# Performance work log

Measured on AMD Instinct MI355X. Metric: run time of the kernel, lower is better.

The kernel has to match this reference:

```python
import jax, jax.numpy as jnp
import numpy as np

N, E, IN, HID, OUT, H = 10000, 320000, 256, 128, 128, 4
SLOPE = 0.2

def setup_inputs() -> dict:
    key = jax.random.key(0)
    ks = jax.random.split(key, 12)
    s = lambda d: 1.0 / np.sqrt(d)
    return {
        "x": jax.random.normal(ks[0], (N, IN), jnp.float32),
        "edge_index": jax.random.randint(ks[1], (2, E), 0, N, jnp.int32),
        "W1": jax.random.normal(ks[2], (IN, H * HID), jnp.float32) * s(IN),
        "a_src1": jax.random.normal(ks[3], (H, HID), jnp.float32) * s(HID),
        "a_dst1": jax.random.normal(ks[4], (H, HID), jnp.float32) * s(HID),
        "b1": jnp.zeros((H * HID,), jnp.float32),
        "W2": jax.random.normal(ks[5], (H * HID, H * OUT), jnp.float32) * s(H * HID),
        "a_src2": jax.random.normal(ks[6], (H, OUT), jnp.float32) * s(OUT),
        "a_dst2": jax.random.normal(ks[7], (H, OUT), jnp.float32) * s(OUT),
        "b2": jnp.zeros((OUT,), jnp.float32),
    }

def _gat_layer(x, src, dst, W, a_src, a_dst, bias, concat, C):
    n = x.shape[0]
    h = (x @ W).reshape(n, H, C)                      # [N,H,C]
    alpha_s = jnp.einsum('nhc,hc->nh', h, a_src)      # [N,H]
    alpha_d = jnp.einsum('nhc,hc->nh', h, a_dst)
    e = jax.nn.leaky_relu(alpha_s[src] + alpha_d[dst], SLOPE)  # [E,H]
    # segment softmax over incoming edges of each dst node
    m = jax.ops.segment_max(e, dst, num_segments=n)   # [N,H]
    m = jnp.where(jnp.isfinite(m), m, 0.0)
    ex = jnp.exp(e - m[dst])
    denom = jax.ops.segment_sum(ex, dst, num_segments=n)
    alpha = ex / (denom[dst] + 1e-16)                 # [E,H]
    msg = h[src] * alpha[:, :, None]                  # [E,H,C]
    out = jax.ops.segment_sum(msg, dst, num_segments=n)  # [N,H,C]
    out = out.reshape(n, H * C) if concat else out.mean(axis=1)
    return out + bias

def reference(x, edge_index, W1, a_src1, a_dst1, b1, W2, a_src2, a_dst2, b2):
    n = x.shape[0]
    loops = jnp.arange(n, dtype=edge_index.dtype)
    src = jnp.concatenate([edge_index[0], loops])
    dst = jnp.concatenate([edge_index[1], loops])
    h = _gat_layer(x, src, dst, W1, a_src1, a_dst1, b1, True, HID)
    h = jax.nn.relu(h)  # dropout is identity in eval mode
    out = _gat_layer(h, src, dst, W2, a_src2, a_dst2, b2, False, OUT)
    return out
```

## Files before the change

### kernel.cpp

```cpp
#include <hip/hip_runtime.h>
#include <hip/hip_fp16.h>
#include <math.h>

#define Nn 10000
#define Ee 320000
#define EE 330000
#define INF_ 256
#define NH 4
#define OUTC 128
#define F1 512
#define F2 512
#define SLOPE 0.2f
#define STRIDE 80
#define LDK 72
#define MT 157

#define TP1_BLOCKS 32
#define TP2_BLOCKS 64
#define ZC_BLOCKS 40
#define P1_GRID (TP1_BLOCKS + ZC_BLOCKS)
#define GEMM_TILES 640
#define SCAT_BLOCKS 430
#define G1_GRID (GEMM_TILES + SCAT_BLOCKS + TP2_BLOCKS)

static __device__ __forceinline__ float lrelu(float x) { return fmaxf(x, SLOPE * x); }

using frag_ab = __attribute__((ext_vector_type(8))) _Float16;
using frag_c  = __attribute__((ext_vector_type(4))) float;

static __device__ __forceinline__ void tile_decode(int bid, int& m, int& h) {
    int m8 = bid & 7, rest = bid >> 3;
    h = rest & 3;
    m = (rest >> 2) * 8 + m8;
}

__global__ __launch_bounds__(256) void prep_w1(int* counts, const float* __restrict__ W1,
                                               _Float16* __restrict__ w1t) {
    __shared__ _Float16 tile[64 * 65];
    int b = blockIdx.x, t = threadIdx.x;
    if (b < TP1_BLOCKS) {
        int k0 = (b >> 3) * 64, n0 = (b & 7) * 64;
        int cl = t & 63, rw = t >> 6;
#pragma unroll
        for (int it = 0; it < 16; it++) {
            int r = it * 4 + rw;
            tile[cl * 65 + r] = (_Float16)W1[(size_t)(k0 + r) * F1 + n0 + cl];
        }
        __syncthreads();
#pragma unroll
        for (int it = 0; it < 16; it++) {
            int nl = it * 4 + rw;
            w1t[(size_t)(n0 + nl) * INF_ + k0 + cl] = tile[nl * 65 + cl];
        }
    } else {
        int i = (b - TP1_BLOCKS) * 256 + t;
        if (i < Nn) counts[i] = 0;
    }
}

template <bool AF32>
static __device__ void gemm_tile(const _Float16* __restrict__ Ah,
                                 const float* __restrict__ Af,
                                 const _Float16* __restrict__ BT,
                                 _Float16* __restrict__ C,
                                 const float* __restrict__ a_src,
                                 const float* __restrict__ a_dst,
                                 float* __restrict__ as_out,
                                 float* __restrict__ ad_out,
                                 int K, int bmi, int head,
                                 _Float16* As, _Float16* Bs) {
    const int tid = threadIdx.x;
    const int wave = tid >> 6, lane = tid & 63;
    const int q = lane >> 4, ml = lane & 15;
    const int bm = bmi * 64, bn = head * 128;
    const int srow = tid >> 2, scol = (tid & 3) * 16;

    frag_c acc[8];
#pragma unroll
    for (int f = 0; f < 8; f++)
#pragma unroll
        for (int r = 0; r < 4; r++) acc[f][r] = 0.f;

    for (int k0 = 0; k0 < K; k0 += 64) {
        int gm = bm + srow;
        frag_ab av0, av1;
        if (gm < Nn) {
            if constexpr (AF32) {
                const float* Ap = Af + (size_t)gm * K + k0 + scol;
                float4 v0 = *(const float4*)Ap;
                float4 v1 = *(const float4*)(Ap + 4);
                float4 v2 = *(const float4*)(Ap + 8);
                float4 v3 = *(const float4*)(Ap + 12);
                av0[0] = (_Float16)v0.x; av0[1] = (_Float16)v0.y;
                av0[2] = (_Float16)v0.z; av0[3] = (_Float16)v0.w;
                av0[4] = (_Float16)v1.x; av0[5] = (_Float16)v1.y;
                av0[6] = (_Float16)v1.z; av0[7] = (_Float16)v1.w;
                av1[0] = (_Float16)v2.x; av1[1] = (_Float16)v2.y;
                av1[2] = (_Float16)v2.z; av1[3] = (_Float16)v2.w;
                av1[4] = (_Float16)v3.x; av1[5] = (_Float16)v3.y;
                av1[6] = (_Float16)v3.z; av1[7] = (_Float16)v3.w;
            } else {
                av0 = *(const frag_ab*)(Ah + (size_t)gm * K + k0 + scol);
                av1 = *(const frag_ab*)(Ah + (size_t)gm * K + k0 + scol + 8);
            }
        } else {
#pragma unroll
            for (int j = 0; j < 8; j++) { av0[j] = (_Float16)0.f; av1[j] = (_Float16)0.f; }
        }
        frag_ab b00 = *(const frag_ab*)(BT + (size_t)(bn + srow) * K + k0 + scol);
        frag_ab b01 = *(const frag_ab*)(BT + (size_t)(bn + srow) * K + k0 + scol + 8);
        frag_ab b10 = *(const frag_ab*)(BT + (size_t)(bn + 64 + srow) * K + k0 + scol);
        frag_ab b11 = *(const frag_ab*)(BT + (size_t)(bn + 64 + srow) * K + k0 + scol + 8);

        *(frag_ab*)&As[srow * LDK + scol]     = av0;
        *(frag_ab*)&As[srow * LDK + scol + 8] = av1;
        *(frag_ab*)&Bs[srow * LDK + scol]     = b00;
        *(frag_ab*)&Bs[srow * LDK + scol + 8] = b01;
        *(frag_ab*)&Bs[(64 + srow) * LDK + scol]     = b10;
        *(frag_ab*)&Bs[(64 + srow) * LDK + scol + 8] = b11;
        __syncthreads();
        frag_ab a0 = *(frag_ab*)&As[(wave * 16 + ml) * LDK + q * 8];
        frag_ab a1 = *(frag_ab*)&As[(wave * 16 + ml) * LDK + 32 + q * 8];
#pragma unroll
        for (int f = 0; f < 8; f++) {
            frag_ab bl = *(frag_ab*)&Bs[(f * 16 + ml) * LDK + q * 8];
            acc[f] = __builtin_amdgcn_mfma_f32_16x16x32_f16(a0, bl, acc[f], 0, 0, 0);
            frag_ab bh = *(frag_ab*)&Bs[(f * 16 + ml) * LDK + 32 + q * 8];
            acc[f] = __builtin_amdgcn_mfma_f32_16x16x32_f16(a1, bh, acc[f], 0, 0, 0);
        }
        __syncthreads();
    }
    float asum[4] = {}, dsum[4] = {};
#pragma unroll
    for (int f = 0; f < 8; f++) {
        int cl = f * 16 + ml;
        int col = bn + cl;
        float sa = a_src[head * 128 + cl];
        float da = a_dst[head * 128 + cl];
#pragma unroll
        for (int r = 0; r < 4; r++) {
            int row = bm + wave * 16 + q * 4 + r;
            if (row < Nn) C[(size_t)row * (NH * 128) + col] = (_Float16)acc[f][r];
            asum[r] += acc[f][r] * sa;
            dsum[r] += acc[f][r] * da;
        }
    }
#pragma unroll
    for (int r = 0; r < 4; r++) {
#pragma unroll
        for (int off = 1; off < 16; off <<= 1) {
            asum[r] += __shfl_xor(asum[r], off);
            dsum[r] += __shfl_xor(dsum[r], off);
        }
    }
    if (ml == 0) {
#pragma unroll
        for (int r = 0; r < 4; r++) {
            int row = bm + wave * 16 + q * 4 + r;
            if (row < Nn) {
                as_out[(size_t)head * Nn + row] = asum[r];
                ad_out[(size_t)head * Nn + row] = dsum[r];
            }
        }
    }
}

__global__ __launch_bounds__(256) void gemm1_scatter(const float* __restrict__ x,
                                                     const _Float16* __restrict__ w1t,
                                                     _Float16* __restrict__ hh,
                                                     const float* __restrict__ a_src,
                                                     const float* __restrict__ a_dst,
                                                     float* __restrict__ as_out,
                                                     float* __restrict__ ad_out,
                                                     const int* __restrict__ ei,
                                                     int* counts, int* __restrict__ csr,
                                                     const float* __restrict__ W2,
                                                     _Float16* __restrict__ w2t) {
    __shared__ _Float16 As[64 * LDK];
    __shared__ _Float16 Bs[128 * LDK];
    int bid = blockIdx.x;
    int t = threadIdx.x;
    if (bid < GEMM_TILES) {
        int m, h;
        tile_decode(bid, m, h);
        if (m < MT)
            gemm_tile<true>(nullptr, x, w1t, hh, a_src, a_dst, as_out, ad_out,
                            INF_, m, h, As, Bs);
    } else if (bid < GEMM_TILES + SCAT_BLOCKS) {
        int bi = bid - GEMM_TILES;
        for (int e = bi * 256 + t; e < EE; e += SCAT_BLOCKS * 256) {
            int src, dst;
            if (e < Ee) { src = ei[e]; dst = ei[Ee + e]; }
            else        { src = e - Ee; dst = e - Ee; }
            int slot = atomicAdd(&counts[dst], 1);
            if (slot < STRIDE) csr[dst * STRIDE + slot] = src;
        }
    } else {
        int bb = bid - GEMM_TILES - SCAT_BLOCKS;
        int k0 = (bb >> 3) * 64, n0 = (bb & 7) * 64;
        int cl = t & 63, r4 = t >> 6;
        _Float16* tile = As;
#pragma unroll
        for (int it = 0; it < 16; it++) {
            int r = it * 4 + r4;
            tile[cl * 65 + r] = (_Float16)W2[(size_t)(k0 + r) * F2 + n0 + cl];
        }
        __syncthreads();
#pragma unroll
        for (int it = 0; it < 16; it++) {
            int nl = it * 4 + r4;
            w2t[(size_t)(n0 + nl) * F1 + k0 + cl] = tile[nl * 65 + cl];
        }
    }
}

__global__ __launch_bounds__(256) void gemm2(const _Float16* __restrict__ aggh,
                                             const _Float16* __restrict__ w2t,
                                             _Float16* __restrict__ hh,
                                             const float* __restrict__ a_src,
                                             const float* __restrict__ a_dst,
                                             float* __restrict__ as_out,
                                             float* __restrict__ ad_out) {
    __shared__ _Float16 As[64 * LDK];
    __shared__ _Float16 Bs[128 * LDK];
    int m, h;
    tile_decode(blockIdx.x, m, h);
    if (m < MT)
        gemm_tile<false>(aggh, nullptr, w2t, hh, a_src, a_dst, as_out, ad_out,
                         F1, m, h, As, Bs);
}

__global__ __launch_bounds__(256) void passAB1(const int* __restrict__ counts,
                                               const int* __restrict__ csr,
                                               const float* __restrict__ as,
                                               const float* __restrict__ ad,
                                               const _Float16* __restrict__ hh,
                                               const float* __restrict__ b1,
                                               _Float16* __restrict__ agg) {
    __shared__ int2 ew[16][84];
    int head = blockIdx.x & 3;
    int qw = threadIdx.x >> 4;
    int l = threadIdx.x & 15;
    int n = (blockIdx.x >> 2) * 16 + qw;
    int deg = counts[n]; if (deg > STRIDE) deg = STRIDE;
    int pdeg = (deg + 7) & ~7;
    const float* ash = as + (size_t)head * Nn;
    float adh = ad[(size_t)head * Nn + n];
    int base = n * STRIDE;
    float s = 0.f;
    for (int k = l; k < pdeg; k += 16) {
        int src = 0; float e = 0.f;
        if (k < deg) {
            src = csr[base + k];
            e = __expf(lrelu(ash[src] + adh));
        }
        ew[qw][k] = make_int2(src, __float_as_int(e));
        s += e;
    }
    s += __shfl_xor(s, 1);
    s += __shfl_xor(s, 2);
    s += __shfl_xor(s, 4);
    s += __shfl_xor(s, 8);
    float inv = 1.f / (s + 1e-16f);
    int c = head * 128 + (l << 3);
    float acc[8] = {};
    for (int kk = 0; kk < pdeg; kk += 8) {
        int2 pj[8];
#pragma unroll
        for (int j = 0; j < 8; j++) pj[j] = ew[qw][kk + j];
#pragma unroll
        for (int j = 0; j < 8; j++) {
            float w = __int_as_float(pj[j].y);
            frag_ab r = *(const frag_ab*)(hh + (size_t)pj[j].x * F1 + c);
#pragma unroll
            for (int u = 0; u < 8; u++) acc[u] = fmaf((float)r[u], w, acc[u]);
        }
    }
    _Float16 oh[8];
#pragma unroll
    for (int j = 0; j < 8; j++)
        oh[j] = (_Float16)fmaxf(acc[j] * inv + b1[c + j], 0.f);
    *(float4*)&agg[(size_t)n * F1 + c] = *(float4*)oh;
}

__global__ __launch_bounds__(256) void passAB2(const int* __restrict__ counts,
                                               const int* __restrict__ csr,
                                               const float* __restrict__ as,
                                               const float* __restrict__ ad,
                                               const _Float16* __restrict__ hh,
                                               _Float16* __restrict__ tmp) {
    __shared__ int2 ew[16][84];
    int head = blockIdx.x & 3;
    int qw = threadIdx.x >> 4;
    int l = threadIdx.x & 15;
    int n = (blockIdx.x >> 2) * 16 + qw;
    int deg = counts[n]; if (deg > STRIDE) deg = STRIDE;
    int pdeg = (deg + 7) & ~7;
    const float* ash = as + (size_t)head * Nn;
    float adh = ad[(size_t)head * Nn + n];
    int base = n * STRIDE;
    float s = 0.f;
    for (int k = l; k < pdeg; k += 16) {
        int src = 0; float e = 0.f;
        if (k < deg) {
            src = csr[base + k];
            e = __expf(lrelu(ash[src] + adh));
        }
        ew[qw][k] = make_int2(src, __float_as_int(e));
        s += e;
    }
    s += __shfl_xor(s, 1);
    s += __shfl_xor(s, 2);
    s += __shfl_xor(s, 4);
    s += __shfl_xor(s, 8);
    float inv = 1.f / (s + 1e-16f);
    int c = head * 128 + (l << 3);
    float acc[8] = {};
    for (int kk = 0; kk < pdeg; kk += 8) {
        int2 pj[8];
#pragma unroll
        for (int j = 0; j < 8; j++) pj[j] = ew[qw][kk + j];
#pragma unroll
        for (int j = 0; j < 8; j++) {
            float w = __int_as_float(pj[j].y);
            frag_ab r = *(const frag_ab*)(hh + (size_t)pj[j].x * F2 + c);
#pragma unroll
            for (int u = 0; u < 8; u++) acc[u] = fmaf((float)r[u], w, acc[u]);
        }
    }
    float qq = 0.25f * inv;
    _Float16 oh[8];
#pragma unroll
    for (int j = 0; j < 8; j++) oh[j] = (_Float16)(acc[j] * qq);
    *(float4*)&tmp[(size_t)n * F2 + c] = *(float4*)oh;
}

__global__ void reduce4(const _Float16* __restrict__ tmp, const float* __restrict__ b2,
                        float* __restrict__ out) {
    int i = blockIdx.x * 256 + threadIdx.x;
    if (i >= Nn * OUTC) return;
    int n = i >> 7, oc = i & 127;
    const _Float16* tp = tmp + (size_t)n * 512 + oc;
    out[i] = (float)tp[0] + (float)tp[128] + (float)tp[256] + (float)tp[384] + b2[oc];
}

extern "C" void kernel_launch(void* const* d_in, const int* in_sizes, int n_in,
                              void* d_out, int out_size, void* d_ws, size_t ws_size,
                              hipStream_t stream) {
    const float* x      = (const float*)d_in[0];
    const int*   ei     = (const int*)d_in[1];
    const float* W1     = (const float*)d_in[2];
    const float* a_src1 = (const float*)d_in[3];
    const float* a_dst1 = (const float*)d_in[4];
    const float* b1     = (const float*)d_in[5];
    const float* W2     = (const float*)d_in[6];
    const float* a_src2 = (const float*)d_in[7];
    const float* a_dst2 = (const float*)d_in[8];
    const float* b2     = (const float*)d_in[9];
    float* out = (float*)d_out;

    char* w = (char*)d_ws;
    _Float16* hh   = (_Float16*)w; w += (size_t)Nn * F1 * 2;
    _Float16* aggh = (_Float16*)w; w += (size_t)Nn * F1 * 2;
    _Float16* tmp  = (_Float16*)w; w += (size_t)Nn * F2 * 2;
    _Float16* w1t  = (_Float16*)w; w += (size_t)F1 * INF_ * 2;
    _Float16* w2t  = (_Float16*)w; w += (size_t)F2 * F1 * 2;
    float* as1     = (float*)w;    w += (size_t)NH * Nn * 4;
    float* ad1     = (float*)w;    w += (size_t)NH * Nn * 4;
    float* as2     = (float*)w;    w += (size_t)NH * Nn * 4;
    float* ad2     = (float*)w;    w += (size_t)NH * Nn * 4;
    int* csr       = (int*)w;      w += (size_t)Nn * STRIDE * 4;
    int* counts    = (int*)w;      w += (size_t)Nn * 4;

    prep_w1<<<P1_GRID, 256, 0, stream>>>(counts, W1, w1t);

    gemm1_scatter<<<G1_GRID, 256, 0, stream>>>(x, w1t, hh, a_src1, a_dst1, as1, ad1,
                                               ei, counts, csr, W2, w2t);
    passAB1<<<(Nn / 16) * NH, 256, 0, stream>>>(counts, csr, as1, ad1, hh, b1, aggh);

    gemm2<<<GEMM_TILES, 256, 0, stream>>>(aggh, w2t, hh, a_src2, a_dst2, as2, ad2);
    passAB2<<<(Nn / 16) * NH, 256, 0, stream>>>(counts, csr, as2, ad2, hh, tmp);
    reduce4<<<(Nn * OUTC + 255) / 256, 256, 0, stream>>>(tmp, b2, out);
}
```

Baseline: 176.7 us.

## Load GEMM MFMA fragments directly from global memory, dropping LDS staging

Each wave now reads its A and B MFMA fragments straight from global memory into registers instead of staging 64x64 tiles in shared memory. This removes both __syncthreads per k-step and frees LDS. K becomes a template parameter so the k-loop can fully unroll. In exchange, all four waves load the same B tile separately and the reads are less coalesced, which raises global/L2 traffic.

```diff
diff --git a/kernel.cpp b/kernel.cpp
--- a/kernel.cpp
+++ b/kernel.cpp
@@ -12,7 +12,6 @@
 #define F2 512
 #define SLOPE 0.2f
 #define STRIDE 80
-#define LDK 72
 #define MT 157
 
 #define TP1_BLOCKS 32
@@ -58,7 +57,7 @@
     }
 }
 
-template <bool AF32>
+template <bool AF32, int K>
 static __device__ void gemm_tile(const _Float16* __restrict__ Ah,
                                  const float* __restrict__ Af,
                                  const _Float16* __restrict__ BT,
@@ -67,13 +66,11 @@
                                  const float* __restrict__ a_dst,
                                  float* __restrict__ as_out,
                                  float* __restrict__ ad_out,
-                                 int K, int bmi, int head,
-                                 _Float16* As, _Float16* Bs) {
+                                 int bmi, int head) {
     const int tid = threadIdx.x;
     const int wave = tid >> 6, lane = tid & 63;
     const int q = lane >> 4, ml = lane & 15;
     const int bm = bmi * 64, bn = head * 128;
-    const int srow = tid >> 2, scol = (tid & 3) * 16;
 
     frag_c acc[8];
 #pragma unroll
@@ -81,55 +78,46 @@
 #pragma unroll
         for (int r = 0; r < 4; r++) acc[f][r] = 0.f;
 
+    const int arow = bm + wave * 16 + ml;
+    const bool rowok = arow < Nn;
+    const float*    Apf = AF32 ? (Af + (size_t)arow * K + q * 8) : nullptr;
+    const _Float16* Aph = AF32 ? nullptr : (Ah + (size_t)arow * K + q * 8);
+    const _Float16* Bp  = BT + (size_t)(bn + ml) * K + q * 8;
+
+#pragma unroll
     for (int k0 = 0; k0 < K; k0 += 64) {
-        int gm = bm + srow;
-        frag_ab av0, av1;
-        if (gm < Nn) {
+        frag_ab a0, a1;
+        if (rowok) {
             if constexpr (AF32) {
-                const float* Ap = Af + (size_t)gm * K + k0 + scol;
-                float4 v0 = *(const float4*)Ap;
-                float4 v1 = *(const float4*)(Ap + 4);
-                float4 v2 = *(const float4*)(Ap + 8);
-                float4 v3 = *(const float4*)(Ap + 12);
-                av0[0] = (_Float16)v0.x; av0[1] = (_Float16)v0.y;
-                av0[2] = (_Float16)v0.z; av0[3] = (_Float16)v0.w;
-                av0[4] = (_Float16)v1.x; av0[5] = (_Float16)v1.y;
-                av0[6] = (_Float16)v1.z; av0[7] = (_Float16)v1.w;
-                av1[0] = (_Float16)v2.x; av1[1] = (_Float16)v2.y;
-                av1[2] = (_Float16)v2.z; av1[3] = (_Float16)v2.w;
-                av1[4] = (_Float16)v3.x; av1[5] = (_Float16)v3.y;
-                av1[6] = (_Float16)v3.z; av1[7] = (_Float16)v3.w;
+                float4 v0 = *(const float4*)(Apf + k0);
+                float4 v1 = *(const float4*)(Apf + k0 + 4);
+                float4 v2 = *(const float4*)(Apf + k0 + 32);
+                float4 v3 = *(const float4*)(Apf + k0 + 36);
+                a0[0] = (_Float16)v0.x; a0[1] = (_Float16)v0.y;
+                a0[2] = (_Float16)v0.z; a0[3] = (_Float16)v0.w;
+                a0[4] = (_Float16)v1.x; a0[5] = (_Float16)v1.y;
+                a0[6] = (_Float16)v1.z; a0[7] = (_Float16)v1.w;
+                a1[0] = (_Float16)v2.x; a1[1] = (_Float16)v2.y;
+                a1[2] = (_Float16)v2.z; a1[3] = (_Float16)v2.w;
+                a1[4] = (_Float16)v3.x; a1[5] = (_Float16)v3.y;
+                a1[6] = (_Float16)v3.z; a1[7] = (_Float16)v3.w;
             } else {
-                av0 = *(const frag_ab*)(Ah + (size_t)gm * K + k0 + scol);
-                av1 = *(const frag_ab*)(Ah + (size_t)gm * K + k0 + scol + 8);
+                a0 = *(const frag_ab*)(Aph + k0);
+                a1 = *(const frag_ab*)(Aph + k0 + 32);
             }
         } else {
 #pragma unroll
-            for (int j = 0; j < 8; j++) { av0[j] = (_Float16)0.f; av1[j] = (_Float16)0.f; }
-        }
-        frag_ab b00 = *(const frag_ab*)(BT + (size_t)(bn + srow) * K + k0 + scol);
-        frag_ab b01 = *(const frag_ab*)(BT + (size_t)(bn + srow) * K + k0 + scol + 8);
-        frag_ab b10 = *(const frag_ab*)(BT + (size_t)(bn + 64 + srow) * K + k0 + scol);
-        frag_ab b11 = *(const frag_ab*)(BT + (size_t)(bn + 64 + srow) * K + k0 + scol + 8);
-
-        *(frag_ab*)&As[srow * LDK + scol]     = av0;
-        *(frag_ab*)&As[srow * LDK + scol + 8] = av1;
-        *(frag_ab*)&Bs[srow * LDK + scol]     = b00;
-        *(frag_ab*)&Bs[srow * LDK + scol + 8] = b01;
-        *(frag_ab*)&Bs[(64 + srow) * LDK + scol]     = b10;
-        *(frag_ab*)&Bs[(64 + srow) * LDK + scol + 8] = b11;
-        __syncthreads();
-        frag_ab a0 = *(frag_ab*)&As[(wave * 16 + ml) * LDK + q * 8];
-        frag_ab a1 = *(frag_ab*)&As[(wave * 16 + ml) * LDK + 32 + q * 8];
+            for (int j = 0; j < 8; j++) { a0[j] = (_Float16)0.f; a1[j] = (_Float16)0.f; }
+        }
 #pragma unroll
         for (int f = 0; f < 8; f++) {
-            frag_ab bl = *(frag_ab*)&Bs[(f * 16 + ml) * LDK + q * 8];
+            frag_ab bl = *(const frag_ab*)(Bp + (size_t)f * 16 * K + k0);
             acc[f] = __builtin_amdgcn_mfma_f32_16x16x32_f16(a0, bl, acc[f], 0, 0, 0);
-            frag_ab bh = *(frag_ab*)&Bs[(f * 16 + ml) * LDK + 32 + q * 8];
+            frag_ab bh = *(const frag_ab*)(Bp + (size_t)f * 16 * K + k0 + 32);
             acc[f] = __builtin_amdgcn_mfma_f32_16x16x32_f16(a1, bh, acc[f], 0, 0, 0);
         }
-        __syncthreads();
-    }
+    }
+
     float asum[4] = {}, dsum[4] = {};
 #pragma unroll
     for (int f = 0; f < 8; f++) {
@@ -176,16 +164,14 @@
                                                      int* counts, int* __restrict__ csr,
                                                      const float* __restrict__ W2,
                                                      _Float16* __restrict__ w2t) {
-    __shared__ _Float16 As[64 * LDK];
-    __shared__ _Float16 Bs[128 * LDK];
+    __shared__ _Float16 tile[64 * 65];
     int bid = blockIdx.x;
     int t = threadIdx.x;
     if (bid < GEMM_TILES) {
         int m, h;
         tile_decode(bid, m, h);
         if (m < MT)
-            gemm_tile<true>(nullptr, x, w1t, hh, a_src, a_dst, as_out, ad_out,
-                            INF_, m, h, As, Bs);
+            gemm_tile<true, INF_>(nullptr, x, w1t, hh, a_src, a_dst, as_out, ad_out, m, h);
     } else if (bid < GEMM_TILES + SCAT_BLOCKS) {
         int bi = bid - GEMM_TILES;
         for (int e = bi * 256 + t; e < EE; e += SCAT_BLOCKS * 256) {
@@ -199,7 +185,6 @@
         int bb = bid - GEMM_TILES - SCAT_BLOCKS;
         int k0 = (bb >> 3) * 64, n0 = (bb & 7) * 64;
         int cl = t & 63, r4 = t >> 6;
-        _Float16* tile = As;
 #pragma unroll
         for (int it = 0; it < 16; it++) {
             int r = it * 4 + r4;
@@ -221,13 +206,10 @@
                                              const float* __restrict__ a_dst,
                                              float* __restrict__ as_out,
                                              float* __restrict__ ad_out) {
-    __shared__ _Float16 As[64 * LDK];
-    __shared__ _Float16 Bs[128 * LDK];
     int m, h;
     tile_decode(blockIdx.x, m, h);
     if (m < MT)
-        gemm_tile<false>(aggh, nullptr, w2t, hh, a_src, a_dst, as_out, ad_out,
-                         F1, m, h, As, Bs);
+        gemm_tile<false, F1>(aggh, nullptr, w2t, hh, a_src, a_dst, as_out, ad_out, m, h);
 }
 
 __global__ __launch_bounds__(256) void passAB1(const int* __restrict__ counts,
```

Measured after the change: 225.9 us. 27.8% more time.
